# Performance work log

Measured on AMD Instinct MI355X. Metric: run time of the kernel, lower is better.

The kernel has to match this reference:

```python
import jax, jax.numpy as jnp
import numpy as np

B, C, H, W = 4, 256, 256, 512
MAXLOAD = 100


def setup_inputs() -> dict:
    key = jax.random.key(0)
    kf, kx, kw, ky, kh = jax.random.split(key, 5)
    features = jax.random.normal(kf, (B, C, H, W), dtype=jnp.float32)
    # ROIs in original-image coords (image is 2048x1024); x0 > 0 so all ROIs are 'valid'
    x0 = jax.random.uniform(kx, (B, MAXLOAD), minval=1.0, maxval=1200.0)
    bw = jax.random.uniform(kw, (B, MAXLOAD), minval=16.0, maxval=800.0)
    x1 = jnp.minimum(x0 + bw, 2047.0)
    y0 = jax.random.uniform(ky, (B, MAXLOAD), minval=1.0, maxval=600.0)
    bh = jax.random.uniform(kh, (B, MAXLOAD), minval=16.0, maxval=400.0)
    y1 = jnp.minimum(y0 + bh, 1023.0)
    rois = jnp.stack([x0, y0, x1, y1], axis=-1).astype(jnp.float32)  # [B, maxLoad, 4]
    return {"features": features, "rois": rois, "shrink_scale": 4,
            "image_height": 1024, "feature_size": 14}


def reference(features, rois, shrink_scale, image_height, feature_size):
    b, c, h, w = features.shape
    max_load = rois.shape[1]
    fs = feature_size
    dscale = float(shrink_scale)

    rois_flat = rois.reshape(-1, 4)                       # [B*maxLoad, 4]
    val_bind = jnp.repeat(jnp.arange(b), max_load)        # indicator; all ROIs valid by construction
    n = rois_flat.shape[0]

    # per-ROI sampling grids in (shrunken) stacked-image coordinates
    ar = jnp.arange(fs, dtype=jnp.float32)
    xx, yy = jnp.meshgrid(ar, ar, indexing='xy')          # [fs, fs]
    biasx = rois_flat[:, 0]
    scalex = rois_flat[:, 2] - rois_flat[:, 0]
    biasy = rois_flat[:, 1] + val_bind.astype(jnp.float32) * float(image_height)
    scaley = rois_flat[:, 3] - rois_flat[:, 1]
    gridxx = (xx[None] / (fs - 1) * scalex[:, None, None] + biasx[:, None, None]) / dscale  # [N, fs, fs]
    gridyy = (yy[None] / (fs - 1) * scaley[:, None, None] + biasy[:, None, None]) / dscale

    # stack batch along height: [C, B*H, W]
    feats = features.transpose(1, 0, 2, 3).reshape(c, b * h, w)
    hb = b * h

    # normalize as in module, then unnormalize per grid_sample(align_corners=False)
    gx = (gridxx / (w - 1) - 0.5) * 2.0
    gy = (gridyy / (hb - 1) - 0.5) * 2.0
    px = ((gx + 1.0) * w - 1.0) * 0.5
    py = ((gy + 1.0) * hb - 1.0) * 0.5
    # padding_mode='border': clip coordinates
    px = jnp.clip(px, 0.0, w - 1.0)
    py = jnp.clip(py, 0.0, hb - 1.0)

    x0f = jnp.floor(px); y0f = jnp.floor(py)
    wx = px - x0f; wy = py - y0f                           # [N, fs, fs]
    x0i = x0f.astype(jnp.int32); y0i = y0f.astype(jnp.int32)
    x1i = jnp.minimum(x0i + 1, w - 1); y1i = jnp.minimum(y0i + 1, hb - 1)

    f00 = feats[:, y0i, x0i]                               # [C, N, fs, fs]
    f01 = feats[:, y0i, x1i]
    f10 = feats[:, y1i, x0i]
    f11 = feats[:, y1i, x1i]
    wxb = wx[None]; wyb = wy[None]
    out = (f00 * (1 - wxb) * (1 - wyb) + f01 * wxb * (1 - wyb)
           + f10 * (1 - wxb) * wyb + f11 * wxb * wyb)      # [C, N, fs, fs]
    out = out.transpose(1, 0, 2, 3)                        # [N, C, fs, fs]
    return out, val_bind
```

## Files before the change

kernel.cpp:

```cpp
#include <hip/hip_runtime.h>

constexpr int B = 4, C = 256, H = 256, W = 512;
constexpr int MAXLOAD = 100, FS = 14;
constexpr int NROI = B * MAXLOAD;
constexpr int HB = B * H;
constexpr int FS2 = FS * FS;
constexpr int MAIN = NROI * C * FS2;
constexpr int MAIN_BLOCKS = MAIN / 256;
constexpr int NXCD = 8;
constexpr int CHUNK = MAIN_BLOCKS / NXCD;

__global__ __launch_bounds__(256) void pooler_kernel(
    const float* __restrict__ feats,
    const float* __restrict__ rois,
    float* __restrict__ out)
{
    int bid = blockIdx.x;

    if (bid >= MAIN_BLOCKS) {
        int t = (bid - MAIN_BLOCKS) * 256 + threadIdx.x;
        if (t < NROI)
            __builtin_nontemporal_store((float)(t / MAXLOAD), &out[MAIN + t]);
        return;
    }

    int wg = (bid % NXCD) * CHUNK + bid / NXCD;
    int e  = wg * 256 + threadIdx.x;

    int pos = e % FS2;
    int qq  = e / FS2;
    int n   = qq % NROI;
    int c   = qq / NROI;
    int fx  = pos % FS;
    int fy  = pos / FS;
    int vb  = n / MAXLOAD;

    float4 roi = reinterpret_cast<const float4*>(rois)[n];
    float scalex = roi.z - roi.x;
    float scaley = roi.w - roi.y;
    float biasx  = roi.x;
    float biasy  = roi.y + (float)vb * 1024.0f;

    float gridx = ((float)fx * (1.0f / 13.0f) * scalex + biasx) * 0.25f;
    float gridy = ((float)fy * (1.0f / 13.0f) * scaley + biasy) * 0.25f;

    float px = gridx * (512.0f / 511.0f) - 0.5f;
    float py = gridy * (1024.0f / 1023.0f) - 0.5f;
    px = fminf(fmaxf(px, 0.0f), (float)(W - 1));
    py = fminf(fmaxf(py, 0.0f), (float)(HB - 1));

    float x0f = floorf(px), y0f = floorf(py);
    float wx = px - x0f, wy = py - y0f;
    int x0 = (int)x0f, y0 = (int)y0f;
    int x1 = min(x0 + 1, W - 1);
    int y1 = min(y0 + 1, HB - 1);

    int cb  = c * (H * W);
    int ro0 = ((y0 >> 8) * (C * H) + (y0 & (H - 1))) * W + cb;
    int ro1 = ((y1 >> 8) * (C * H) + (y1 & (H - 1))) * W + cb;

    float f00 = feats[ro0 + x0];
    float f01 = feats[ro0 + x1];
    float f10 = feats[ro1 + x0];
    float f11 = feats[ro1 + x1];

    float v0 = f00 + wx * (f01 - f00);
    float v1 = f10 + wx * (f11 - f10);
    float res = v0 + wy * (v1 - v0);

    int out_idx = (n * C + c) * FS2 + pos;
    __builtin_nontemporal_store(res, &out[out_idx]);
}

extern "C" void kernel_launch(void* const* d_in, const int* in_sizes, int n_in,
                              void* d_out, int out_size, void* d_ws, size_t ws_size,
                              hipStream_t stream) {
    const float* feats = (const float*)d_in[0];
    const float* rois  = (const float*)d_in[1];
    float* out = (float*)d_out;

    int tail_blocks = (NROI + 255) / 256;
    pooler_kernel<<<MAIN_BLOCKS + tail_blocks, 256, 0, stream>>>(feats, rois, out);
}
```

Before: 720.8 us.

## Stage ROI feature row segments in shared memory with double buffering

Each block now handles one (channel, ROI) pair. It loads the contiguous horizontal span of the needed feature rows into shared memory, two output rows at a time, with double buffering. A small subset of threads then does the bilinear interpolation from LDS. This aims to replace scattered global gathers with coalesced row loads, at the cost of reading extra unused pixels, low thread utilization during compute, and per-step barriers.

```diff
diff --git a/kernel.cpp b/kernel.cpp
--- a/kernel.cpp
+++ b/kernel.cpp
@@ -6,17 +6,19 @@
 constexpr int HB = B * H;
 constexpr int FS2 = FS * FS;
 constexpr int MAIN = NROI * C * FS2;
-constexpr int MAIN_BLOCKS = MAIN / 256;
+constexpr int MAIN_BLOCKS = C * NROI;
 constexpr int NXCD = 8;
 constexpr int CHUNK = MAIN_BLOCKS / NXCD;
+constexpr int SEGW = 514;
 
 __global__ __launch_bounds__(256) void pooler_kernel(
     const float* __restrict__ feats,
     const float* __restrict__ rois,
     float* __restrict__ out)
 {
+    __shared__ float buf[2][4][SEGW];
+
     int bid = blockIdx.x;
-
     if (bid >= MAIN_BLOCKS) {
         int t = (bid - MAIN_BLOCKS) * 256 + threadIdx.x;
         if (t < NROI)
@@ -25,15 +27,9 @@
     }
 
     int wg = (bid % NXCD) * CHUNK + bid / NXCD;
-    int e  = wg * 256 + threadIdx.x;
-
-    int pos = e % FS2;
-    int qq  = e / FS2;
-    int n   = qq % NROI;
-    int c   = qq / NROI;
-    int fx  = pos % FS;
-    int fy  = pos / FS;
-    int vb  = n / MAXLOAD;
+    int c  = wg / NROI;
+    int n  = wg - c * NROI;
+    int vb = n / MAXLOAD;
 
     float4 roi = reinterpret_cast<const float4*>(rois)[n];
     float scalex = roi.z - roi.x;
@@ -41,35 +37,65 @@
     float biasx  = roi.x;
     float biasy  = roi.y + (float)vb * 1024.0f;
 
-    float gridx = ((float)fx * (1.0f / 13.0f) * scalex + biasx) * 0.25f;
-    float gridy = ((float)fy * (1.0f / 13.0f) * scaley + biasy) * 0.25f;
+    float px_lo = fminf(fmaxf(((0.0f  * (1.0f/13.0f) * scalex + biasx) * 0.25f)
+                              * (512.0f/511.0f) - 0.5f, 0.0f), (float)(W - 1));
+    float px_hi = fminf(fmaxf(((13.0f * (1.0f/13.0f) * scalex + biasx) * 0.25f)
+                              * (512.0f/511.0f) - 0.5f, 0.0f), (float)(W - 1));
+    int x_start = (int)floorf(px_lo);
+    int x_end   = min((int)floorf(px_hi) + 1, W - 1);
+    int seg     = x_end - x_start + 1;
 
-    float px = gridx * (512.0f / 511.0f) - 0.5f;
-    float py = gridy * (1024.0f / 1023.0f) - 0.5f;
-    px = fminf(fmaxf(px, 0.0f), (float)(W - 1));
-    py = fminf(fmaxf(py, 0.0f), (float)(HB - 1));
+    int cHW      = c * (H * W);
+    int out_base = (n * C + c) * FS2;
 
-    float x0f = floorf(px), y0f = floorf(py);
-    float wx = px - x0f, wy = py - y0f;
-    int x0 = (int)x0f, y0 = (int)y0f;
-    int x1 = min(x0 + 1, W - 1);
-    int y1 = min(y0 + 1, HB - 1);
+    int tid  = threadIdx.x;
+    int j    = tid >> 6;
+    int lane = tid & 63;
 
-    int cb  = c * (H * W);
-    int ro0 = ((y0 >> 8) * (C * H) + (y0 & (H - 1))) * W + cb;
-    int ro1 = ((y1 >> 8) * (C * H) + (y1 & (H - 1))) * W + cb;
+    auto stage = [&](int q, int qb) {
+        int fy = 2 * q + (j >> 1);
+        float gy = ((float)fy * (1.0f/13.0f) * scaley + biasy) * 0.25f;
+        float py = fminf(fmaxf(gy * (1024.0f/1023.0f) - 0.5f, 0.0f), (float)(HB - 1));
+        int y0 = (int)floorf(py);
+        int y  = (j & 1) ? min(y0 + 1, HB - 1) : y0;
+        int base = ((y >> 8) * (C * H) + (y & (H - 1))) * W + cHW + x_start;
+        for (int k = lane; k < seg; k += 64)
+            buf[qb][j][k] = feats[base + k];
+    };
 
-    float f00 = feats[ro0 + x0];
-    float f01 = feats[ro0 + x1];
-    float f10 = feats[ro1 + x0];
-    float f11 = feats[ro1 + x1];
+    stage(0, 0);
+    __syncthreads();
 
-    float v0 = f00 + wx * (f01 - f00);
-    float v1 = f10 + wx * (f11 - f10);
-    float res = v0 + wy * (v1 - v0);
+    for (int p = 0; p < 7; ++p) {
+        if (p < 6) stage(p + 1, (p + 1) & 1);
 
-    int out_idx = (n * C + c) * FS2 + pos;
-    __builtin_nontemporal_store(res, &out[out_idx]);
+        if (tid < 28) {
+            int half = tid / 14;
+            int fx   = tid - half * 14;
+            int fy   = 2 * p + half;
+
+            float gx  = ((float)fx * (1.0f/13.0f) * scalex + biasx) * 0.25f;
+            float gyv = ((float)fy * (1.0f/13.0f) * scaley + biasy) * 0.25f;
+            float px = fminf(fmaxf(gx  * (512.0f/511.0f)  - 0.5f, 0.0f), (float)(W - 1));
+            float py = fminf(fmaxf(gyv * (1024.0f/1023.0f) - 0.5f, 0.0f), (float)(HB - 1));
+
+            float x0f = floorf(px), y0f = floorf(py);
+            float wx = px - x0f,  wy = py - y0f;
+            int i0 = (int)x0f - x_start;
+            int i1 = min((int)x0f + 1, W - 1) - x_start;
+
+            const float* r0 = buf[p & 1][half * 2 + 0];
+            const float* r1 = buf[p & 1][half * 2 + 1];
+            float f00 = r0[i0], f01 = r0[i1];
+            float f10 = r1[i0], f11 = r1[i1];
+
+            float v0 = f00 + wx * (f01 - f00);
+            float v1 = f10 + wx * (f11 - f10);
+            float res = v0 + wy * (v1 - v0);
+            __builtin_nontemporal_store(res, &out[out_base + fy * FS + fx]);
+        }
+        __syncthreads();
+    }
 }
 
 extern "C" void kernel_launch(void* const* d_in, const int* in_sizes, int n_in,
```

After: 1.044 ms. +44.8%, slower.
